# Kernel optimization log

Hardware: AMD Instinct MI355X
Metric: run time of the kernel (lower is better)

The kernel has to match this reference:

```python
import jax, jax.numpy as jnp
import numpy as np

D, H, E = 1024, 2048, 16  # input_dim, expert hidden (2*D), num_experts
B, S = 4, 2048
TEMP = 1.0
LN_EPS = 1e-5


def setup_inputs() -> dict:
    key = jax.random.key(0)
    ks = jax.random.split(key, 8)
    x = jax.random.normal(ks[0], (B, S, D), dtype=jnp.float32)
    router_w = 0.02 * jax.random.normal(ks[1], (E, D), dtype=jnp.float32)  # nn.Linear(D,E,bias=False)
    w1 = 0.02 * jax.random.normal(ks[2], (E, H, D), dtype=jnp.float32)     # torch Linear weight [out,in]
    b1 = jnp.zeros((E, H), dtype=jnp.float32)
    ln_g = jnp.ones((E, H), dtype=jnp.float32)
    ln_b = jnp.zeros((E, H), dtype=jnp.float32)
    w2 = 0.02 * jax.random.normal(ks[3], (E, D, H), dtype=jnp.float32)
    b2 = jnp.zeros((E, D), dtype=jnp.float32)
    return {"x": x, "router_w": router_w, "w1": w1, "b1": b1,
            "ln_g": ln_g, "ln_b": ln_b, "w2": w2, "b2": b2}


def reference(x, router_w, w1, b1, ln_g, ln_b, w2, b2):
    d = x.shape[-1]
    xf = x.reshape(-1, d)                       # [T, D]
    logits = (xf @ router_w.T) / TEMP           # [T, E]
    dispatch = jax.nn.softmax(logits, axis=0)   # softmax over tokens
    combine = jax.nn.softmax(logits, axis=-1)   # softmax over experts
    slots = dispatch.T @ xf                     # [E, D] one slot per expert
    # per-expert MLP, vectorized over E: Linear -> LayerNorm -> GELU -> Linear
    h = jnp.einsum('ed,ehd->eh', slots, w1) + b1          # [E, H]
    mu = h.mean(-1, keepdims=True)
    var = ((h - mu) ** 2).mean(-1, keepdims=True)         # biased var (torch LayerNorm)
    h = (h - mu) * jax.lax.rsqrt(var + LN_EPS) * ln_g + ln_b
    h = jax.nn.gelu(h, approximate=False)                 # nn.GELU exact erf
    slot_out = jnp.einsum('eh,edh->ed', h, w2) + b2       # [E, D]
    out = combine @ slot_out                              # [T, D]
    # router aux loss and entropy (eval-mode state subset)
    mean_usage = combine.mean(0)                          # [E]
    p = jax.nn.softmax(router_w.mean(-1), axis=0)         # [E]
    n_exp = router_w.shape[0]
    router_loss = n_exp * (mean_usage * p).sum()
    entropy = -(combine * jnp.log(combine + 1e-8)).sum(-1).mean()
    return out.reshape(x.shape), router_loss, entropy
```

## Files before the change

### kernel.cpp

```cpp
#include <hip/hip_runtime.h>
#include <hip/hip_bf16.h>
#include <math.h>

#define T_ 8192
#define D_ 1024
#define E_ 16
#define H_ 2048

__device__ __forceinline__ float wave_sum(float v) {
    #pragma unroll
    for (int m = 32; m >= 1; m >>= 1) v += __shfl_xor(v, m, 64);
    return v;
}
__device__ __forceinline__ float wave_max(float v) {
    #pragma unroll
    for (int m = 32; m >= 1; m >>= 1) v = fmaxf(v, __shfl_xor(v, m, 64));
    return v;
}

__global__ __launch_bounds__(256) void k1_logits(const float* __restrict__ x,
                                                 const float* __restrict__ rw,
                                                 float* __restrict__ logits) {
    __shared__ float rw_lds[E_ * D_];
    for (int i = threadIdx.x; i < E_ * D_; i += 256) rw_lds[i] = rw[i];
    __syncthreads();
    const int wave = threadIdx.x >> 6, lane = threadIdx.x & 63;
    const int t0 = blockIdx.x * 32 + wave * 8;
    const float4* rl = (const float4*)rw_lds;
    for (int ti = 0; ti < 8; ++ti) {
        const int t = t0 + ti;
        const float4* xr = (const float4*)(x + (size_t)t * D_);
        float4 xv[4];
        #pragma unroll
        for (int k = 0; k < 4; ++k) xv[k] = xr[lane + 64 * k];
        float my = 0.0f;
        #pragma unroll
        for (int e = 0; e < E_; ++e) {
            float s = 0.0f;
            #pragma unroll
            for (int k = 0; k < 4; ++k) {
                float4 wv = rl[e * 256 + lane + 64 * k];
                s += xv[k].x * wv.x + xv[k].y * wv.y + xv[k].z * wv.z + xv[k].w * wv.w;
            }
            s = wave_sum(s);
            if (lane == e) my = s;
        }
        if (lane < E_) logits[(size_t)t * E_ + lane] = my;
    }
}

__global__ __launch_bounds__(256) void k2a_colstats(const float* __restrict__ logits,
                                                    float* __restrict__ colmax,
                                                    float* __restrict__ colsum) {
    const int e = blockIdx.x, tid = threadIdx.x;
    float m = -1e30f;
    for (int t = tid; t < T_; t += 256) m = fmaxf(m, logits[(size_t)t * E_ + e]);
    m = wave_max(m);
    __shared__ float red[4];
    if ((tid & 63) == 0) red[tid >> 6] = m;
    __syncthreads();
    m = fmaxf(fmaxf(red[0], red[1]), fmaxf(red[2], red[3]));
    __syncthreads();
    float s = 0.0f;
    for (int t = tid; t < T_; t += 256) s += expf(logits[(size_t)t * E_ + e] - m);
    s = wave_sum(s);
    if ((tid & 63) == 0) red[tid >> 6] = s;
    __syncthreads();
    if (tid == 0) {
        colmax[e] = m;
        colsum[e] = red[0] + red[1] + red[2] + red[3];
    }
}

__global__ __launch_bounds__(256) void k2b_combine(const float* __restrict__ logits,
                                                   float* __restrict__ combine,
                                                   float* __restrict__ musum,
                                                   float* __restrict__ entacc) {
    const int t = blockIdx.x * 256 + threadIdx.x;
    const int lane = threadIdx.x & 63;
    float l[E_];
    const float4* lr = (const float4*)(logits + (size_t)t * E_);
    #pragma unroll
    for (int q = 0; q < 4; ++q) {
        float4 v = lr[q];
        l[q * 4 + 0] = v.x; l[q * 4 + 1] = v.y; l[q * 4 + 2] = v.z; l[q * 4 + 3] = v.w;
    }
    float m = l[0];
    #pragma unroll
    for (int e = 1; e < E_; ++e) m = fmaxf(m, l[e]);
    float s = 0.0f;
    float c[E_];
    #pragma unroll
    for (int e = 0; e < E_; ++e) { c[e] = expf(l[e] - m); s += c[e]; }
    const float inv = 1.0f / s;
    float ent = 0.0f;
    #pragma unroll
    for (int e = 0; e < E_; ++e) {
        c[e] *= inv;
        ent -= c[e] * logf(c[e] + 1e-8f);
    }
    float4* cw = (float4*)(combine + (size_t)t * E_);
    #pragma unroll
    for (int q = 0; q < 4; ++q) {
        float4 v = { c[q * 4 + 0], c[q * 4 + 1], c[q * 4 + 2], c[q * 4 + 3] };
        cw[q] = v;
    }
    #pragma unroll
    for (int e = 0; e < E_; ++e) {
        float v = wave_sum(c[e]);
        if (lane == 0) atomicAdd(&musum[e], v);
    }
    float ev = wave_sum(ent);
    if (lane == 0) atomicAdd(entacc, ev);
}

__global__ __launch_bounds__(256) void k3_slots(const float* __restrict__ x,
                                                const float* __restrict__ logits,
                                                const float* __restrict__ colmax,
                                                const float* __restrict__ colsum,
                                                float* __restrict__ slots) {
    const int tid = threadIdx.x;
    __shared__ float disp[128 * E_];
    __shared__ float cm[E_], cs[E_];
    if (tid < E_) { cm[tid] = colmax[tid]; cs[tid] = 1.0f / colsum[tid]; }
    __syncthreads();
    const int t0 = blockIdx.y * 128;
    for (int idx = tid; idx < 128 * E_; idx += 256) {
        const int tt = idx >> 4, e = idx & 15;
        disp[idx] = expf(logits[(size_t)(t0 + tt) * E_ + e] - cm[e]) * cs[e];
    }
    __syncthreads();
    const int d = blockIdx.x * 256 + tid;
    float acc[E_];
    #pragma unroll
    for (int e = 0; e < E_; ++e) acc[e] = 0.0f;
    const float* xp = x + (size_t)t0 * D_ + d;
    for (int tt = 0; tt < 128; ++tt) {
        const float xv = xp[(size_t)tt * D_];
        const float* dr = &disp[tt * E_];
        #pragma unroll
        for (int e = 0; e < E_; ++e) acc[e] += dr[e] * xv;
    }
    #pragma unroll
    for (int e = 0; e < E_; ++e) atomicAdd(&slots[e * D_ + d], acc[e]);
}

__global__ __launch_bounds__(256) void k4_h(const float* __restrict__ slots,
                                            const float* __restrict__ w1,
                                            const float* __restrict__ b1,
                                            float* __restrict__ h) {
    const int e = blockIdx.x >> 9;
    const int jbase = (blockIdx.x & 511) * 4;
    __shared__ float sl[D_];
    for (int i = threadIdx.x; i < D_; i += 256) sl[i] = slots[e * D_ + i];
    __syncthreads();
    const int wave = threadIdx.x >> 6, lane = threadIdx.x & 63;
    const int j = jbase + wave;
    const float4* wr = (const float4*)(w1 + ((size_t)e * H_ + j) * D_);
    const float4* sr = (const float4*)sl;
    float s = 0.0f;
    #pragma unroll
    for (int k = 0; k < 4; ++k) {
        float4 wv = wr[lane + 64 * k];
        float4 sv = sr[lane + 64 * k];
        s += wv.x * sv.x + wv.y * sv.y + wv.z * sv.z + wv.w * sv.w;
    }
    s = wave_sum(s);
    if (lane == 0) h[e * H_ + j] = s + b1[e * H_ + j];
}

__global__ __launch_bounds__(256) void k5_ln_gelu(const float* __restrict__ h,
                                                  const float* __restrict__ g,
                                                  const float* __restrict__ bb,
                                                  float* __restrict__ h2) {
    const int e = blockIdx.x, tid = threadIdx.x;
    float v[8];
    float s = 0.0f, ss = 0.0f;
    #pragma unroll
    for (int k = 0; k < 8; ++k) {
        v[k] = h[e * H_ + tid + 256 * k];
        s += v[k]; ss += v[k] * v[k];
    }
    s = wave_sum(s); ss = wave_sum(ss);
    __shared__ float rs[4], rss[4];
    if ((tid & 63) == 0) { rs[tid >> 6] = s; rss[tid >> 6] = ss; }
    __syncthreads();
    s = rs[0] + rs[1] + rs[2] + rs[3];
    ss = rss[0] + rss[1] + rss[2] + rss[3];
    const float mean = s * (1.0f / H_);
    const float var = ss * (1.0f / H_) - mean * mean;
    const float rstd = rsqrtf(var + 1e-5f);
    #pragma unroll
    for (int k = 0; k < 8; ++k) {
        const int i = tid + 256 * k;
        float y = (v[k] - mean) * rstd * g[e * H_ + i] + bb[e * H_ + i];
        h2[e * H_ + i] = 0.5f * y * (1.0f + erff(y * 0.70710678118654752f));
    }
}

__global__ __launch_bounds__(256) void k6_slotout(const float* __restrict__ h2,
                                                  const float* __restrict__ w2,
                                                  const float* __restrict__ b2,
                                                  float* __restrict__ slot_out) {
    const int e = blockIdx.x >> 8;
    const int dbase = (blockIdx.x & 255) * 4;
    __shared__ float hl[H_];
    for (int i = threadIdx.x; i < H_; i += 256) hl[i] = h2[e * H_ + i];
    __syncthreads();
    const int wave = threadIdx.x >> 6, lane = threadIdx.x & 63;
    const int d = dbase + wave;
    const float4* wr = (const float4*)(w2 + ((size_t)e * D_ + d) * H_);
    const float4* hr = (const float4*)hl;
    float s = 0.0f;
    #pragma unroll
    for (int k = 0; k < 8; ++k) {
        float4 wv = wr[lane + 64 * k];
        float4 hv = hr[lane + 64 * k];
        s += wv.x * hv.x + wv.y * hv.y + wv.z * hv.z + wv.w * hv.w;
    }
    s = wave_sum(s);
    if (lane == 0) slot_out[e * D_ + d] = s + b2[e * D_ + d];
}

__global__ __launch_bounds__(256) void k7_out(const float* __restrict__ combine,
                                              const float* __restrict__ slot_out,
                                              float* __restrict__ out) {
    const int tbase = blockIdx.x * 16;
    __shared__ float cl[256];
    cl[threadIdx.x] = combine[(size_t)tbase * E_ + threadIdx.x];
    __syncthreads();
    float4 so[E_];
    const float4* sr = (const float4*)slot_out;
    #pragma unroll
    for (int e = 0; e < E_; ++e) so[e] = sr[e * 256 + threadIdx.x];
    for (int tt = 0; tt < 16; ++tt) {
        float4 acc = { 0.0f, 0.0f, 0.0f, 0.0f };
        #pragma unroll
        for (int e = 0; e < E_; ++e) {
            const float c = cl[tt * E_ + e];
            acc.x += c * so[e].x; acc.y += c * so[e].y;
            acc.z += c * so[e].z; acc.w += c * so[e].w;
        }
        ((float4*)out)[(size_t)(tbase + tt) * 256 + threadIdx.x] = acc;
    }
}

__global__ __launch_bounds__(256) void k8_scalars(const float* __restrict__ rw,
                                                  const float* __restrict__ musum,
                                                  const float* __restrict__ entacc,
                                                  float* __restrict__ out_scalars) {
    const int tid = threadIdx.x, lane = tid & 63, wave = tid >> 6;
    __shared__ float red[4];
    __shared__ float rm[E_];
    for (int e = 0; e < E_; ++e) {
        float s = 0.0f;
        for (int i = tid; i < D_; i += 256) s += rw[e * D_ + i];
        s = wave_sum(s);
        if (lane == 0) red[wave] = s;
        __syncthreads();
        if (tid == 0) rm[e] = (red[0] + red[1] + red[2] + red[3]) * (1.0f / D_);
        __syncthreads();
    }
    if (tid == 0) {
        float m = rm[0];
        for (int e = 1; e < E_; ++e) m = fmaxf(m, rm[e]);
        float s = 0.0f, pe[E_];
        for (int e = 0; e < E_; ++e) { pe[e] = expf(rm[e] - m); s += pe[e]; }
        float loss = 0.0f;
        for (int e = 0; e < E_; ++e) loss += (musum[e] * (1.0f / T_)) * (pe[e] / s);
        loss *= (float)E_;
        out_scalars[0] = loss;
        out_scalars[1] = entacc[0] * (1.0f / T_);
    }
}

extern "C" void kernel_launch(void* const* d_in, const int* in_sizes, int n_in,
                              void* d_out, int out_size, void* d_ws, size_t ws_size,
                              hipStream_t stream) {
    const float* x    = (const float*)d_in[0];
    const float* rw   = (const float*)d_in[1];
    const float* w1   = (const float*)d_in[2];
    const float* b1   = (const float*)d_in[3];
    const float* ln_g = (const float*)d_in[4];
    const float* ln_b = (const float*)d_in[5];
    const float* w2   = (const float*)d_in[6];
    const float* b2   = (const float*)d_in[7];

    float* out = (float*)d_out;
    float* wsf = (float*)d_ws;

    float* logits   = wsf;
    float* combine  = wsf + 131072;
    float* colmax   = wsf + 262144;
    float* colsum   = wsf + 262160;
    float* h        = wsf + 262176;
    float* h2       = wsf + 294944;
    float* slot_out = wsf + 327712;
    float* slots    = wsf + 344096;
    float* musum    = wsf + 360480;
    float* entacc   = wsf + 360496;

    hipMemsetAsync(slots, 0, (size_t)(16384 + 16 + 1) * sizeof(float), stream);

    k1_logits<<<T_ / 32, 256, 0, stream>>>(x, rw, logits);
    k2a_colstats<<<E_, 256, 0, stream>>>(logits, colmax, colsum);
    k2b_combine<<<T_ / 256, 256, 0, stream>>>(logits, combine, musum, entacc);
    k3_slots<<<dim3(4, 64), 256, 0, stream>>>(x, logits, colmax, colsum, slots);
    k4_h<<<E_ * 512, 256, 0, stream>>>(slots, w1, b1, h);
    k5_ln_gelu<<<E_, 256, 0, stream>>>(h, ln_g, ln_b, h2);
    k6_slotout<<<E_ * 256, 256, 0, stream>>>(h2, w2, b2, slot_out);
    k7_out<<<T_ / 16, 256, 0, stream>>>(combine, slot_out, out);
    k8_scalars<<<1, 256, 0, stream>>>(rw, musum, entacc, out + (size_t)T_ * D_);
}
```

Measured before the change: 448.4 us.

## Fuse combine softmax into logits kernel and restructure expert GEMV kernels

The per-token combine softmax, entropy and usage sums are now computed inside the logits kernel using 16-lane shuffles, which removes the separate combine kernel and its re-read of logits. The expert GEMV kernels now make each wave handle four rows, keep the slot or hidden vector in registers instead of LDS, and use nontemporal loads for the weight streams, with four times fewer blocks. The slots kernel reads dispatch weights as float4, and the scalars kernel reduces router rows one wave per expert instead of in a loop with barriers. The risks are fewer blocks in flight for the weight-bound GEMVs and per-wave atomics in the fused kernel.

```diff
diff --git a/kernel.cpp b/kernel.cpp
--- a/kernel.cpp
+++ b/kernel.cpp
@@ -7,6 +7,8 @@
 #define E_ 16
 #define H_ 2048
 
+typedef float f4 __attribute__((ext_vector_type(4)));
+
 __device__ __forceinline__ float wave_sum(float v) {
     #pragma unroll
     for (int m = 32; m >= 1; m >>= 1) v += __shfl_xor(v, m, 64);
@@ -17,16 +19,30 @@
     for (int m = 32; m >= 1; m >>= 1) v = fmaxf(v, __shfl_xor(v, m, 64));
     return v;
 }
-
-__global__ __launch_bounds__(256) void k1_logits(const float* __restrict__ x,
-                                                 const float* __restrict__ rw,
-                                                 float* __restrict__ logits) {
+__device__ __forceinline__ float grp16_sum(float v) {
+    #pragma unroll
+    for (int m = 8; m >= 1; m >>= 1) v += __shfl_xor(v, m, 16);
+    return v;
+}
+__device__ __forceinline__ float grp16_max(float v) {
+    #pragma unroll
+    for (int m = 8; m >= 1; m >>= 1) v = fmaxf(v, __shfl_xor(v, m, 16));
+    return v;
+}
+
+__global__ __launch_bounds__(256) void k1_logits_combine(const float* __restrict__ x,
+                                                         const float* __restrict__ rw,
+                                                         float* __restrict__ logits,
+                                                         float* __restrict__ combine,
+                                                         float* __restrict__ musum,
+                                                         float* __restrict__ entacc) {
     __shared__ float rw_lds[E_ * D_];
     for (int i = threadIdx.x; i < E_ * D_; i += 256) rw_lds[i] = rw[i];
     __syncthreads();
     const int wave = threadIdx.x >> 6, lane = threadIdx.x & 63;
     const int t0 = blockIdx.x * 32 + wave * 8;
     const float4* rl = (const float4*)rw_lds;
+    float mu_reg = 0.0f, ent_reg = 0.0f;
     for (int ti = 0; ti < 8; ++ti) {
         const int t = t0 + ti;
         const float4* xr = (const float4*)(x + (size_t)t * D_);
@@ -46,7 +62,20 @@
             if (lane == e) my = s;
         }
         if (lane < E_) logits[(size_t)t * E_ + lane] = my;
-    }
+        float m = grp16_max(my);
+        float cexp = expf(my - m);
+        float ssum = grp16_sum(cexp);
+        float c = cexp / ssum;
+        if (lane < E_) {
+            combine[(size_t)t * E_ + lane] = c;
+            mu_reg += c;
+        }
+        float entc = (lane < E_) ? (-c * logf(c + 1e-8f)) : 0.0f;
+        entc = grp16_sum(entc);
+        if (lane == 0) ent_reg += entc;
+    }
+    if (lane < E_) atomicAdd(&musum[lane], mu_reg);
+    if (lane == 0) atomicAdd(entacc, ent_reg);
 }
 
 __global__ __launch_bounds__(256) void k2a_colstats(const float* __restrict__ logits,
@@ -72,48 +101,6 @@
     }
 }
 
-__global__ __launch_bounds__(256) void k2b_combine(const float* __restrict__ logits,
-                                                   float* __restrict__ combine,
-                                                   float* __restrict__ musum,
-                                                   float* __restrict__ entacc) {
-    const int t = blockIdx.x * 256 + threadIdx.x;
-    const int lane = threadIdx.x & 63;
-    float l[E_];
-    const float4* lr = (const float4*)(logits + (size_t)t * E_);
-    #pragma unroll
-    for (int q = 0; q < 4; ++q) {
-        float4 v = lr[q];
-        l[q * 4 + 0] = v.x; l[q * 4 + 1] = v.y; l[q * 4 + 2] = v.z; l[q * 4 + 3] = v.w;
-    }
-    float m = l[0];
-    #pragma unroll
-    for (int e = 1; e < E_; ++e) m = fmaxf(m, l[e]);
-    float s = 0.0f;
-    float c[E_];
-    #pragma unroll
-    for (int e = 0; e < E_; ++e) { c[e] = expf(l[e] - m); s += c[e]; }
-    const float inv = 1.0f / s;
-    float ent = 0.0f;
-    #pragma unroll
-    for (int e = 0; e < E_; ++e) {
-        c[e] *= inv;
-        ent -= c[e] * logf(c[e] + 1e-8f);
-    }
-    float4* cw = (float4*)(combine + (size_t)t * E_);
-    #pragma unroll
-    for (int q = 0; q < 4; ++q) {
-        float4 v = { c[q * 4 + 0], c[q * 4 + 1], c[q * 4 + 2], c[q * 4 + 3] };
-        cw[q] = v;
-    }
-    #pragma unroll
-    for (int e = 0; e < E_; ++e) {
-        float v = wave_sum(c[e]);
-        if (lane == 0) atomicAdd(&musum[e], v);
-    }
-    float ev = wave_sum(ent);
-    if (lane == 0) atomicAdd(entacc, ev);
-}
-
 __global__ __launch_bounds__(256) void k3_slots(const float* __restrict__ x,
                                                 const float* __restrict__ logits,
                                                 const float* __restrict__ colmax,
@@ -137,9 +124,12 @@
     const float* xp = x + (size_t)t0 * D_ + d;
     for (int tt = 0; tt < 128; ++tt) {
         const float xv = xp[(size_t)tt * D_];
-        const float* dr = &disp[tt * E_];
-        #pragma unroll
-        for (int e = 0; e < E_; ++e) acc[e] += dr[e] * xv;
+        const float4* dr = (const float4*)&disp[tt * E_];
+        float4 d0 = dr[0], d1 = dr[1], d2 = dr[2], d3 = dr[3];
+        acc[0]  += d0.x * xv; acc[1]  += d0.y * xv; acc[2]  += d0.z * xv; acc[3]  += d0.w * xv;
+        acc[4]  += d1.x * xv; acc[5]  += d1.y * xv; acc[6]  += d1.z * xv; acc[7]  += d1.w * xv;
+        acc[8]  += d2.x * xv; acc[9]  += d2.y * xv; acc[10] += d2.z * xv; acc[11] += d2.w * xv;
+        acc[12] += d3.x * xv; acc[13] += d3.y * xv; acc[14] += d3.z * xv; acc[15] += d3.w * xv;
     }
     #pragma unroll
     for (int e = 0; e < E_; ++e) atomicAdd(&slots[e * D_ + d], acc[e]);
@@ -149,24 +139,26 @@
                                             const float* __restrict__ w1,
                                             const float* __restrict__ b1,
                                             float* __restrict__ h) {
-    const int e = blockIdx.x >> 9;
-    const int jbase = (blockIdx.x & 511) * 4;
-    __shared__ float sl[D_];
-    for (int i = threadIdx.x; i < D_; i += 256) sl[i] = slots[e * D_ + i];
-    __syncthreads();
+    const int e = blockIdx.x >> 7;
+    const int jgrp = (blockIdx.x & 127) * 16;
     const int wave = threadIdx.x >> 6, lane = threadIdx.x & 63;
-    const int j = jbase + wave;
-    const float4* wr = (const float4*)(w1 + ((size_t)e * H_ + j) * D_);
-    const float4* sr = (const float4*)sl;
-    float s = 0.0f;
-    #pragma unroll
-    for (int k = 0; k < 4; ++k) {
-        float4 wv = wr[lane + 64 * k];
-        float4 sv = sr[lane + 64 * k];
-        s += wv.x * sv.x + wv.y * sv.y + wv.z * sv.z + wv.w * sv.w;
-    }
-    s = wave_sum(s);
-    if (lane == 0) h[e * H_ + j] = s + b1[e * H_ + j];
+    const float4* sr = (const float4*)(slots + e * D_);
+    float4 sv[4];
+    #pragma unroll
+    for (int k = 0; k < 4; ++k) sv[k] = sr[lane + 64 * k];
+    #pragma unroll
+    for (int r = 0; r < 4; ++r) {
+        const int j = jgrp + wave * 4 + r;
+        const f4* wr = (const f4*)(w1 + ((size_t)e * H_ + j) * D_);
+        float s = 0.0f;
+        #pragma unroll
+        for (int k = 0; k < 4; ++k) {
+            f4 wv = __builtin_nontemporal_load(&wr[lane + 64 * k]);
+            s += wv.x * sv[k].x + wv.y * sv[k].y + wv.z * sv[k].z + wv.w * sv[k].w;
+        }
+        s = wave_sum(s);
+        if (lane == 0) h[e * H_ + j] = s + b1[e * H_ + j];
+    }
 }
 
 __global__ __launch_bounds__(256) void k5_ln_gelu(const float* __restrict__ h,
@@ -202,24 +194,26 @@
                                                   const float* __restrict__ w2,
                                                   const float* __restrict__ b2,
                                                   float* __restrict__ slot_out) {
-    const int e = blockIdx.x >> 8;
-    const int dbase = (blockIdx.x & 255) * 4;
-    __shared__ float hl[H_];
-    for (int i = threadIdx.x; i < H_; i += 256) hl[i] = h2[e * H_ + i];
-    __syncthreads();
+    const int e = blockIdx.x >> 6;
+    const int dgrp = (blockIdx.x & 63) * 16;
     const int wave = threadIdx.x >> 6, lane = threadIdx.x & 63;
-    const int d = dbase + wave;
-    const float4* wr = (const float4*)(w2 + ((size_t)e * D_ + d) * H_);
-    const float4* hr = (const float4*)hl;
-    float s = 0.0f;
-    #pragma unroll
-    for (int k = 0; k < 8; ++k) {
-        float4 wv = wr[lane + 64 * k];
-        float4 hv = hr[lane + 64 * k];
-        s += wv.x * hv.x + wv.y * hv.y + wv.z * hv.z + wv.w * hv.w;
-    }
-    s = wave_sum(s);
-    if (lane == 0) slot_out[e * D_ + d] = s + b2[e * D_ + d];
+    const float4* hr = (const float4*)(h2 + e * H_);
+    float4 hv[8];
+    #pragma unroll
+    for (int k = 0; k < 8; ++k) hv[k] = hr[lane + 64 * k];
+    #pragma unroll
+    for (int r = 0; r < 4; ++r) {
+        const int d = dgrp + wave * 4 + r;
+        const f4* wr = (const f4*)(w2 + ((size_t)e * D_ + d) * H_);
+        float s = 0.0f;
+        #pragma unroll
+        for (int k = 0; k < 8; ++k) {
+            f4 wv = __builtin_nontemporal_load(&wr[lane + 64 * k]);
+            s += wv.x * hv[k].x + wv.y * hv[k].y + wv.z * hv[k].z + wv.w * hv[k].w;
+        }
+        s = wave_sum(s);
+        if (lane == 0) slot_out[e * D_ + d] = s + b2[e * D_ + d];
+    }
 }
 
 __global__ __launch_bounds__(256) void k7_out(const float* __restrict__ combine,
@@ -250,17 +244,21 @@
                                                   const float* __restrict__ entacc,
                                                   float* __restrict__ out_scalars) {
     const int tid = threadIdx.x, lane = tid & 63, wave = tid >> 6;
-    __shared__ float red[4];
     __shared__ float rm[E_];
-    for (int e = 0; e < E_; ++e) {
+    #pragma unroll
+    for (int q = 0; q < 4; ++q) {
+        const int e = wave * 4 + q;
+        const float4* rr = (const float4*)(rw + e * D_);
         float s = 0.0f;
-        for (int i = tid; i < D_; i += 256) s += rw[e * D_ + i];
+        #pragma unroll
+        for (int k = 0; k < 4; ++k) {
+            float4 v = rr[lane * 4 + k];
+            s += v.x + v.y + v.z + v.w;
+        }
         s = wave_sum(s);
-        if (lane == 0) red[wave] = s;
-        __syncthreads();
-        if (tid == 0) rm[e] = (red[0] + red[1] + red[2] + red[3]) * (1.0f / D_);
-        __syncthreads();
-    }
+        if (lane == 0) rm[e] = s * (1.0f / D_);
+    }
+    __syncthreads();
     if (tid == 0) {
         float m = rm[0];
         for (int e = 1; e < E_; ++e) m = fmaxf(m, rm[e]);
@@ -300,15 +298,14 @@
     float* musum    = wsf + 360480;
     float* entacc   = wsf + 360496;
 
-    hipMemsetAsync(slots, 0, (size_t)(16384 + 16 + 1) * sizeof(float), stream);
-
-    k1_logits<<<T_ / 32, 256, 0, stream>>>(x, rw, logits);
+    (void)hipMemsetAsync(slots, 0, (size_t)(16384 + 16 + 1) * sizeof(float), stream);
+
+    k1_logits_combine<<<T_ / 32, 256, 0, stream>>>(x, rw, logits, combine, musum, entacc);
     k2a_colstats<<<E_, 256, 0, stream>>>(logits, colmax, colsum);
-    k2b_combine<<<T_ / 256, 256, 0, stream>>>(logits, combine, musum, entacc);
     k3_slots<<<dim3(4, 64), 256, 0, stream>>>(x, logits, colmax, colsum, slots);
-    k4_h<<<E_ * 512, 256, 0, stream>>>(slots, w1, b1, h);
+    k4_h<<<E_ * 128, 256, 0, stream>>>(slots, w1, b1, h);
     k5_ln_gelu<<<E_, 256, 0, stream>>>(h, ln_g, ln_b, h2);
-    k6_slotout<<<E_ * 256, 256, 0, stream>>>(h2, w2, b2, slot_out);
+    k6_slotout<<<E_ * 64, 256, 0, stream>>>(h2, w2, b2, slot_out);
     k7_out<<<T_ / 16, 256, 0, stream>>>(combine, slot_out, out);
     k8_scalars<<<1, 256, 0, stream>>>(rw, musum, entacc, out + (size_t)T_ * D_);
 }
```

Result: faster. 388.7 us (-13.3%).
